# Performance work log

Measured on AMD Instinct MI355X. Metric: run time of the kernel, lower is better.

## Reference

```python
import jax, jax.numpy as jnp
import numpy as np

B, N, D, H = 4, 2048, 256, 8
DH = D // H

def setup_inputs() -> dict:
    key = jax.random.key(0)
    ks = jax.random.split(key, 7)
    s = 1.0 / np.sqrt(DH)
    return {
        "sequences": jax.random.normal(ks[0], (B, N, D), dtype=jnp.float32),
        "Wq": jax.random.uniform(ks[1], (H, DH, DH), jnp.float32, -s, s),
        "bq": jax.random.uniform(ks[2], (H, DH), jnp.float32, -s, s),
        "Wk": jax.random.uniform(ks[3], (H, DH, DH), jnp.float32, -s, s),
        "bk": jax.random.uniform(ks[4], (H, DH), jnp.float32, -s, s),
        "Wv": jax.random.uniform(ks[5], (H, DH, DH), jnp.float32, -s, s),
        "bv": jax.random.uniform(ks[6], (H, DH), jnp.float32, -s, s),
    }

def reference(sequences, Wq, bq, Wk, bk, Wv, bv):
    # sequences: [B, N, D] -> [B, N, H, DH] (head h sees columns h*DH:(h+1)*DH)
    x = sequences.reshape(B, N, H, DH)
    # per-head Linear: y = x @ W.T + b
    q = jnp.einsum("bnhd,hed->bnhe", x, Wq) + bq
    k = jnp.einsum("bnhd,hed->bnhe", x, Wk) + bk
    v = jnp.einsum("bnhd,hed->bnhe", x, Wv) + bv
    scores = jnp.einsum("bnhe,bmhe->bhnm", q, k) / jnp.sqrt(jnp.float32(DH))
    attn = jax.nn.softmax(scores, axis=-1)  # [B, H, N, N]
    out = jnp.einsum("bhnm,bmhe->bnhe", attn, v)
    # hstack of per-head results == concat over last dim == reshape
    return out.reshape(B, N, D)
```

## Files before the change

kernel.cpp:

```cpp
#include <hip/hip_runtime.h>
#include <hip/hip_bf16.h>

typedef __bf16 bf16;
typedef __bf16 bf16x8 __attribute__((ext_vector_type(8)));
typedef __bf16 bf16x4 __attribute__((ext_vector_type(4)));
typedef float  f32x4  __attribute__((ext_vector_type(4)));

#define B_  4
#define N_  2048
#define D_  256
#define H_  8
#define DH_ 32
#define QKV_ELEMS (B_*H_*N_*DH_)

#define QSC    (0.17677669529663687f * 1.4426950408889634f)
#define NBIAS  (-17.312340490667562f)

#if __has_builtin(__builtin_amdgcn_exp2f)
__device__ inline float exp2_hw(float x) { return __builtin_amdgcn_exp2f(x); }
#else
__device__ inline float exp2_hw(float x) {
    float r; asm volatile("v_exp_f32 %0, %1" : "=v"(r) : "v"(x)); return r;
}
#endif

__device__ inline bf16x8 ldcvt8(const float* __restrict__ p) {
    f32x4 a = *(const f32x4*)p;
    f32x4 b = *(const f32x4*)(p + 4);
    bf16x8 r;
    r[0] = (bf16)a[0]; r[1] = (bf16)a[1]; r[2] = (bf16)a[2]; r[3] = (bf16)a[3];
    r[4] = (bf16)b[0]; r[5] = (bf16)b[1]; r[6] = (bf16)b[2]; r[7] = (bf16)b[3];
    return r;
}

__global__ __launch_bounds__(256, 4) void qkv_proj_kernel(
    const float* __restrict__ x,
    const float* __restrict__ Wq, const float* __restrict__ bq,
    const float* __restrict__ Wk, const float* __restrict__ bk,
    const float* __restrict__ Wv, const float* __restrict__ bv,
    bf16* __restrict__ Qg, bf16* __restrict__ Kg, bf16* __restrict__ Vg)
{
    const int nt8 = blockIdx.x & 7, bh = blockIdx.x >> 3;
    const int h   = bh & (H_-1),   b  = bh >> 3;
    const int wave = threadIdx.x >> 6, lane = threadIdx.x & 63;
    const int l16 = lane & 15, q4 = lane >> 4;

    bf16x8 wqf[2], wkf[2], wvf[2];
    f32x4  bq4[2], bk4[2];
    float  bvs[2];
    #pragma unroll
    for (int half = 0; half < 2; ++half) {
        wqf[half] = ldcvt8(Wq + (h*DH_ + half*16 + l16)*DH_ + q4*8);
        wkf[half] = ldcvt8(Wk + (h*DH_ + half*16 + l16)*DH_ + q4*8);
        wvf[half] = ldcvt8(Wv + (h*DH_ + half*16 + l16)*DH_ + q4*8);
        bq4[half] = *(const f32x4*)(bq + h*DH_ + half*16 + q4*4);
        bk4[half] = *(const f32x4*)(bk + h*DH_ + half*16 + q4*4);
        bvs[half] = bv[h*DH_ + half*16 + l16];
    }

    const f32x4 z = {0.f,0.f,0.f,0.f};
    #pragma unroll
    for (int it = 0; it < 4; ++it) {
        const int n0 = nt8*256 + it*64 + wave*16;
        bf16x8 xf = ldcvt8(x + ((size_t)(b*N_ + n0 + l16))*D_ + h*DH_ + q4*8);

        #pragma unroll
        for (int half = 0; half < 2; ++half) {
            f32x4 dq = __builtin_amdgcn_mfma_f32_16x16x32_bf16(wqf[half], xf, z, 0, 0, 0);
            f32x4 dk = __builtin_amdgcn_mfma_f32_16x16x32_bf16(wkf[half], xf, z, 0, 0, 0);
            f32x4 dv = __builtin_amdgcn_mfma_f32_16x16x32_bf16(xf, wvf[half], z, 0, 0, 0);
            bf16x4 pq, pk, pv;
            #pragma unroll
            for (int r = 0; r < 4; ++r) {
                pq[r] = (bf16)((dq[r] + bq4[half][r]) * QSC);
                pk[r] = (bf16)(dk[r] + bk4[half][r]);
                pv[r] = (bf16)(dv[r] + bvs[half]);
            }
            const size_t row = ((size_t)bh*N_ + n0 + l16)*DH_ + half*16 + q4*4;
            *(bf16x4*)(Qg + row) = pq;
            *(bf16x4*)(Kg + row) = pk;
            const int e = half*16 + l16;
            const size_t idx = ((size_t)bh << 16) + ((size_t)(n0 >> 5) << 10)
                             + (e << 5) + (q4 << 3) + (((n0 >> 4) & 1) << 2);
            *(bf16x4*)(Vg + idx) = pv;
        }
    }
}

__global__ __launch_bounds__(256, 4) void attn_kernel(
    const bf16* __restrict__ Qg, const bf16* __restrict__ Kg,
    const bf16* __restrict__ Vg, float* __restrict__ out)
{
    const int qt = blockIdx.x & 31;
    const int bh = blockIdx.x >> 5;
    const int h  = bh & (H_-1), b = bh >> 3;
    const int lane = threadIdx.x & 63;
    const int wave = threadIdx.x >> 6;
    const int l16 = lane & 15, q4 = lane >> 4;

    __shared__ bf16 Klds[2][128*DH_];

    const bf16* Kb = Kg + (size_t)bh*N_*DH_;
    const bf16* Vb = Vg + ((size_t)bh << 16);
    const int qrow0 = qt*64 + wave*16;

    bf16x8 qb = *(const bf16x8*)(Qg + ((size_t)bh*N_ + qrow0 + l16)*DH_ + q4*8);

    bf16x8 ones;
    #pragma unroll
    for (int j = 0; j < 8; ++j) ones[j] = (bf16)1.0f;

    f32x4 ot0 = {0,0,0,0}, ot1 = {0,0,0,0}, osum = {0,0,0,0};
    const f32x4 zb = {NBIAS, NBIAS, NBIAS, NBIAS};

    const int soff = wave*1024 + lane*8;

    {
        bf16x8 s0 = *(const bf16x8*)(Kb + soff);
        bf16x8 s1 = *(const bf16x8*)(Kb + soff + 512);
        *(bf16x8*)(&Klds[0][soff])       = s0;
        *(bf16x8*)(&Klds[0][soff + 512]) = s1;
    }
    __syncthreads();

    for (int kt = 0; kt < 16; ++kt) {
        const int cur = kt & 1, nxt = cur ^ 1, nkt = (kt + 1) & 15;

        const bf16* gn = Kb + (size_t)nkt*4096 + soff;
        bf16x8 ks0 = *(const bf16x8*)gn;
        bf16x8 ks1 = *(const bf16x8*)(gn + 512);

        f32x4 st[8];
        #pragma unroll
        for (int kc = 0; kc < 8; ++kc) {
            bf16x8 kf = *(const bf16x8*)(&Klds[cur][(kc*16 + l16)*DH_ + q4*8]);
            st[kc] = __builtin_amdgcn_mfma_f32_16x16x32_bf16(kf, qb, zb, 0, 0, 0);
        }

        bf16x8 vf[8];
        const bf16* Vc = Vb + (size_t)kt*128*DH_;
        #pragma unroll
        for (int i = 0; i < 8; ++i)
            vf[i] = *(const bf16x8*)(Vc + (size_t)(i >> 1)*1024 + ((i & 1)*16 + l16)*32 + q4*8);

        #pragma unroll
        for (int kk = 0; kk < 4; ++kk) {
            bf16x8 pb;
            #pragma unroll
            for (int half = 0; half < 2; ++half)
                #pragma unroll
                for (int r = 0; r < 4; ++r)
                    pb[half*4 + r] = (bf16)exp2_hw(st[kk*2 + half][r]);
            ot0  = __builtin_amdgcn_mfma_f32_16x16x32_bf16(vf[kk*2 + 0], pb, ot0, 0, 0, 0);
            ot1  = __builtin_amdgcn_mfma_f32_16x16x32_bf16(vf[kk*2 + 1], pb, ot1, 0, 0, 0);
            osum = __builtin_amdgcn_mfma_f32_16x16x32_bf16(ones, pb, osum, 0, 0, 0);
        }

        *(bf16x8*)(&Klds[nxt][soff])       = ks0;
        *(bf16x8*)(&Klds[nxt][soff + 512]) = ks1;
        __syncthreads();
    }

    const float inv = 1.0f / osum[0];
    #pragma unroll
    for (int dhh = 0; dhh < 2; ++dhh) {
        const f32x4& o = dhh ? ot1 : ot0;
        f32x4 w;
        #pragma unroll
        for (int r = 0; r < 4; ++r) w[r] = o[r] * inv;
        *(f32x4*)(out + ((size_t)b*N_ + qrow0 + l16)*D_ + h*DH_ + dhh*16 + q4*4) = w;
    }
}

extern "C" void kernel_launch(void* const* d_in, const int* in_sizes, int n_in,
                              void* d_out, int out_size, void* d_ws, size_t ws_size,
                              hipStream_t stream)
{
    const float* x  = (const float*)d_in[0];
    const float* Wq = (const float*)d_in[1];
    const float* bq = (const float*)d_in[2];
    const float* Wk = (const float*)d_in[3];
    const float* bk = (const float*)d_in[4];
    const float* Wv = (const float*)d_in[5];
    const float* bv = (const float*)d_in[6];
    float* out = (float*)d_out;

    bf16* Qg = (bf16*)d_ws;
    bf16* Kg = Qg + QKV_ELEMS;
    bf16* Vg = Kg + QKV_ELEMS;

    qkv_proj_kernel<<<dim3(B_*H_*8), dim3(256), 0, stream>>>(
        x, Wq, bq, Wk, bk, Wv, bv, Qg, Kg, Vg);
    attn_kernel<<<dim3(B_*H_*(N_/64)), dim3(256), 0, stream>>>(Qg, Kg, Vg, out);
}
```

Baseline: 118.6 us.

## Stage V tiles through LDS and widen QKV projection grid

The attention kernel now double-buffers V in shared memory alongside K, with contiguous 16-element-per-thread cooperative loads. The per-wave V fragments come from LDS instead of direct global loads, and each 128-key tile is split into two 64-key halves to reduce live score registers. The projection kernel launches four times as many blocks, each handling one 64-row chunk instead of looping four times, to raise parallelism. The trade-offs are doubled LDS use, which may cut occupancy, and more repeated weight loads in the projection.

```diff
diff --git a/kernel.cpp b/kernel.cpp
--- a/kernel.cpp
+++ b/kernel.cpp
@@ -40,10 +40,11 @@
     const float* __restrict__ Wv, const float* __restrict__ bv,
     bf16* __restrict__ Qg, bf16* __restrict__ Kg, bf16* __restrict__ Vg)
 {
-    const int nt8 = blockIdx.x & 7, bh = blockIdx.x >> 3;
-    const int h   = bh & (H_-1),   b  = bh >> 3;
+    const int nt = blockIdx.x & 31, bh = blockIdx.x >> 5;
+    const int h  = bh & (H_-1),    b  = bh >> 3;
     const int wave = threadIdx.x >> 6, lane = threadIdx.x & 63;
     const int l16 = lane & 15, q4 = lane >> 4;
+    const int n0 = nt*64 + wave*16;
 
     bf16x8 wqf[2], wkf[2], wvf[2];
     f32x4  bq4[2], bk4[2];
@@ -58,32 +59,28 @@
         bvs[half] = bv[h*DH_ + half*16 + l16];
     }
 
+    bf16x8 xf = ldcvt8(x + ((size_t)(b*N_ + n0 + l16))*D_ + h*DH_ + q4*8);
     const f32x4 z = {0.f,0.f,0.f,0.f};
-    #pragma unroll
-    for (int it = 0; it < 4; ++it) {
-        const int n0 = nt8*256 + it*64 + wave*16;
-        bf16x8 xf = ldcvt8(x + ((size_t)(b*N_ + n0 + l16))*D_ + h*DH_ + q4*8);
-
+
+    #pragma unroll
+    for (int half = 0; half < 2; ++half) {
+        f32x4 dq = __builtin_amdgcn_mfma_f32_16x16x32_bf16(wqf[half], xf, z, 0, 0, 0);
+        f32x4 dk = __builtin_amdgcn_mfma_f32_16x16x32_bf16(wkf[half], xf, z, 0, 0, 0);
+        f32x4 dv = __builtin_amdgcn_mfma_f32_16x16x32_bf16(xf, wvf[half], z, 0, 0, 0);
+        bf16x4 pq, pk, pv;
         #pragma unroll
-        for (int half = 0; half < 2; ++half) {
-            f32x4 dq = __builtin_amdgcn_mfma_f32_16x16x32_bf16(wqf[half], xf, z, 0, 0, 0);
-            f32x4 dk = __builtin_amdgcn_mfma_f32_16x16x32_bf16(wkf[half], xf, z, 0, 0, 0);
-            f32x4 dv = __builtin_amdgcn_mfma_f32_16x16x32_bf16(xf, wvf[half], z, 0, 0, 0);
-            bf16x4 pq, pk, pv;
-            #pragma unroll
-            for (int r = 0; r < 4; ++r) {
-                pq[r] = (bf16)((dq[r] + bq4[half][r]) * QSC);
-                pk[r] = (bf16)(dk[r] + bk4[half][r]);
-                pv[r] = (bf16)(dv[r] + bvs[half]);
-            }
-            const size_t row = ((size_t)bh*N_ + n0 + l16)*DH_ + half*16 + q4*4;
-            *(bf16x4*)(Qg + row) = pq;
-            *(bf16x4*)(Kg + row) = pk;
-            const int e = half*16 + l16;
-            const size_t idx = ((size_t)bh << 16) + ((size_t)(n0 >> 5) << 10)
-                             + (e << 5) + (q4 << 3) + (((n0 >> 4) & 1) << 2);
-            *(bf16x4*)(Vg + idx) = pv;
+        for (int r = 0; r < 4; ++r) {
+            pq[r] = (bf16)((dq[r] + bq4[half][r]) * QSC);
+            pk[r] = (bf16)(dk[r] + bk4[half][r]);
+            pv[r] = (bf16)(dv[r] + bvs[half]);
         }
+        const size_t row = ((size_t)bh*N_ + n0 + l16)*DH_ + half*16 + q4*4;
+        *(bf16x4*)(Qg + row) = pq;
+        *(bf16x4*)(Kg + row) = pk;
+        const int e = half*16 + l16;
+        const size_t idx = ((size_t)bh << 16) + ((size_t)(n0 >> 5) << 10)
+                         + (e << 5) + (q4 << 3) + (((n0 >> 4) & 1) << 2);
+        *(bf16x4*)(Vg + idx) = pv;
     }
 }
 
@@ -94,11 +91,13 @@
     const int qt = blockIdx.x & 31;
     const int bh = blockIdx.x >> 5;
     const int h  = bh & (H_-1), b = bh >> 3;
-    const int lane = threadIdx.x & 63;
-    const int wave = threadIdx.x >> 6;
+    const int t    = threadIdx.x;
+    const int lane = t & 63;
+    const int wave = t >> 6;
     const int l16 = lane & 15, q4 = lane >> 4;
 
-    __shared__ bf16 Klds[2][128*DH_];
+    __shared__ bf16 Kl[2][128*DH_];
+    __shared__ bf16 Vl[2][128*DH_];
 
     const bf16* Kb = Kg + (size_t)bh*N_*DH_;
     const bf16* Vb = Vg + ((size_t)bh << 16);
@@ -113,51 +112,57 @@
     f32x4 ot0 = {0,0,0,0}, ot1 = {0,0,0,0}, osum = {0,0,0,0};
     const f32x4 zb = {NBIAS, NBIAS, NBIAS, NBIAS};
 
-    const int soff = wave*1024 + lane*8;
-
     {
-        bf16x8 s0 = *(const bf16x8*)(Kb + soff);
-        bf16x8 s1 = *(const bf16x8*)(Kb + soff + 512);
-        *(bf16x8*)(&Klds[0][soff])       = s0;
-        *(bf16x8*)(&Klds[0][soff + 512]) = s1;
+        bf16x8 k0 = *(const bf16x8*)(Kb + t*16);
+        bf16x8 k1 = *(const bf16x8*)(Kb + t*16 + 8);
+        bf16x8 v0 = *(const bf16x8*)(Vb + t*16);
+        bf16x8 v1 = *(const bf16x8*)(Vb + t*16 + 8);
+        *(bf16x8*)(&Kl[0][t*16])     = k0;
+        *(bf16x8*)(&Kl[0][t*16 + 8]) = k1;
+        *(bf16x8*)(&Vl[0][t*16])     = v0;
+        *(bf16x8*)(&Vl[0][t*16 + 8]) = v1;
     }
     __syncthreads();
 
     for (int kt = 0; kt < 16; ++kt) {
         const int cur = kt & 1, nxt = cur ^ 1, nkt = (kt + 1) & 15;
 
-        const bf16* gn = Kb + (size_t)nkt*4096 + soff;
-        bf16x8 ks0 = *(const bf16x8*)gn;
-        bf16x8 ks1 = *(const bf16x8*)(gn + 512);
-
-        f32x4 st[8];
+        const bf16* gk = Kb + (size_t)nkt*4096 + t*16;
+        const bf16* gv = Vb + (size_t)nkt*4096 + t*16;
+        bf16x8 ka0 = *(const bf16x8*)gk;
+        bf16x8 ka1 = *(const bf16x8*)(gk + 8);
+        bf16x8 va0 = *(const bf16x8*)gv;
+        bf16x8 va1 = *(const bf16x8*)(gv + 8);
+
         #pragma unroll
-        for (int kc = 0; kc < 8; ++kc) {
-            bf16x8 kf = *(const bf16x8*)(&Klds[cur][(kc*16 + l16)*DH_ + q4*8]);
-            st[kc] = __builtin_amdgcn_mfma_f32_16x16x32_bf16(kf, qb, zb, 0, 0, 0);
+        for (int hh = 0; hh < 2; ++hh) {
+            f32x4 st4[4];
+            #pragma unroll
+            for (int kc = 0; kc < 4; ++kc) {
+                bf16x8 kf = *(const bf16x8*)(&Kl[cur][(hh*64 + kc*16 + l16)*DH_ + q4*8]);
+                st4[kc] = __builtin_amdgcn_mfma_f32_16x16x32_bf16(kf, qb, zb, 0, 0, 0);
+            }
+            #pragma unroll
+            for (int kk = 0; kk < 2; ++kk) {
+                bf16x8 pb;
+                #pragma unroll
+                for (int hf = 0; hf < 2; ++hf)
+                    #pragma unroll
+                    for (int r = 0; r < 4; ++r)
+                        pb[hf*4 + r] = (bf16)exp2_hw(st4[kk*2 + hf][r]);
+                const int g = hh*2 + kk;
+                bf16x8 v0 = *(const bf16x8*)(&Vl[cur][g*1024 + l16*DH_ + q4*8]);
+                bf16x8 v1 = *(const bf16x8*)(&Vl[cur][g*1024 + (16 + l16)*DH_ + q4*8]);
+                ot0  = __builtin_amdgcn_mfma_f32_16x16x32_bf16(v0, pb, ot0, 0, 0, 0);
+                ot1  = __builtin_amdgcn_mfma_f32_16x16x32_bf16(v1, pb, ot1, 0, 0, 0);
+                osum = __builtin_amdgcn_mfma_f32_16x16x32_bf16(ones, pb, osum, 0, 0, 0);
+            }
         }
 
-        bf16x8 vf[8];
-        const bf16* Vc = Vb + (size_t)kt*128*DH_;
-        #pragma unroll
-        for (int i = 0; i < 8; ++i)
-            vf[i] = *(const bf16x8*)(Vc + (size_t)(i >> 1)*1024 + ((i & 1)*16 + l16)*32 + q4*8);
-
-        #pragma unroll
-        for (int kk = 0; kk < 4; ++kk) {
-            bf16x8 pb;
-            #pragma unroll
-            for (int half = 0; half < 2; ++half)
-                #pragma unroll
-                for (int r = 0; r < 4; ++r)
-                    pb[half*4 + r] = (bf16)exp2_hw(st[kk*2 + half][r]);
-            ot0  = __builtin_amdgcn_mfma_f32_16x16x32_bf16(vf[kk*2 + 0], pb, ot0, 0, 0, 0);
-            ot1  = __builtin_amdgcn_mfma_f32_16x16x32_bf16(vf[kk*2 + 1], pb, ot1, 0, 0, 0);
-            osum = __builtin_amdgcn_mfma_f32_16x16x32_bf16(ones, pb, osum, 0, 0, 0);
-        }
-
-        *(bf16x8*)(&Klds[nxt][soff])       = ks0;
-        *(bf16x8*)(&Klds[nxt][soff + 512]) = ks1;
+        *(bf16x8*)(&Kl[nxt][t*16])     = ka0;
+        *(bf16x8*)(&Kl[nxt][t*16 + 8]) = ka1;
+        *(bf16x8*)(&Vl[nxt][t*16])     = va0;
+        *(bf16x8*)(&Vl[nxt][t*16 + 8]) = va1;
         __syncthreads();
     }
 
@@ -189,7 +194,7 @@
     bf16* Kg = Qg + QKV_ELEMS;
     bf16* Vg = Kg + QKV_ELEMS;
 
-    qkv_proj_kernel<<<dim3(B_*H_*8), dim3(256), 0, stream>>>(
+    qkv_proj_kernel<<<dim3(B_*H_*32), dim3(256), 0, stream>>>(
         x, Wq, bq, Wk, bk, Wv, bv, Qg, Kg, Vg);
     attn_kernel<<<dim3(B_*H_*(N_/64)), dim3(256), 0, stream>>>(Qg, Kg, Vg, out);
 }
```

Result: faster. 105.6 us (-10.9%).
